# Optimization experiments

Hardware: AMD Instinct MI355X
Metric: run time of the kernel (lower is better)

Reference implementation:

```python
import jax, jax.numpy as jnp
import numpy as np

E = 19   # electrodes
H = 32   # lstm hidden dim per direction


def setup_inputs() -> dict:
    key = jax.random.key(0)
    ks = jax.random.split(key, 8)
    B, T = 64, 2048
    s = 1.0 / np.sqrt(H)  # PyTorch LSTM/Linear init scale
    u = lambda k, shp: jax.random.uniform(k, shp, jnp.float32, -s, s)
    return {
        "x": jax.random.normal(ks[0], (B, T, E), jnp.float32),
        # per-electrode, per-direction LSTM params (input_dim=1 so w_ih is a vector per gate block)
        "w_ih": u(ks[1], (E, 2, 4 * H)),          # [E, dir, 4H]
        "w_hh": u(ks[2], (E, 2, 4 * H, H)),       # [E, dir, 4H, H]
        "b_ih": u(ks[3], (E, 2, 4 * H)),
        "b_hh": u(ks[4], (E, 2, 4 * H)),
        "ln_gamma": jnp.ones((E, 2 * H), jnp.float32),
        "ln_beta": jnp.zeros((E, 2 * H), jnp.float32),
        "fc_w": u(ks[5], (1, 2 * H)),
        "fc_b": u(ks[6], (1,)),
    }


def reference(x, w_ih, w_hh, b_ih, b_hh, ln_gamma, ln_beta, fc_w, fc_b):
    B, T, E_ = x.shape
    # dir 0 = forward time, dir 1 = reversed time (bidirectional)
    xs = jnp.stack([x, x[:, ::-1, :]], axis=-1)      # [B, T, E, 2]
    xs = jnp.moveaxis(xs, 1, 0)                      # [T, B, E, 2]
    b = b_ih + b_hh                                  # [E, 2, 4H]

    h0 = jnp.zeros((B, E_, 2, H), x.dtype)
    c0 = jnp.zeros_like(h0)

    def step(carry, xt):
        h, c = carry
        # xt: [B, E, 2] scalar input per electrode/direction (input_dim == 1)
        gates = xt[..., None] * w_ih + jnp.einsum('bedh,edgh->bedg', h, w_hh) + b
        i, f, g, o = jnp.split(gates, 4, axis=-1)    # PyTorch gate order i,f,g,o
        c = jax.nn.sigmoid(f) * c + jax.nn.sigmoid(i) * jnp.tanh(g)
        h = jax.nn.sigmoid(o) * jnp.tanh(c)
        return (h, c), None

    (hT, _), _ = jax.lax.scan(step, (h0, c0), xs)
    # final hidden: dir0 = fwd at t=T-1 (hn[-2]), dir1 = bwd at t=0 (hn[-1]); concat features
    out = hT.reshape(B, E_, 2 * H)                   # [B, E, 64]

    # per-electrode LayerNorm over the 64-dim feature
    mu = out.mean(-1, keepdims=True)
    var = out.var(-1, keepdims=True)
    out = (out - mu) / jnp.sqrt(var + 1e-5) * ln_gamma + ln_beta

    pooled = out.mean(axis=1)                        # mean over electrodes -> [B, 64]
    logits = pooled @ fc_w.T + fc_b                  # [B, 1]
    return logits[:, 0]
```

## Files before the change

### kernel.cpp

```cpp
#include <hip/hip_runtime.h>
#include <math.h>
#include <stdint.h>

#define E_N 19
#define H_N 32
#define T_N 2048
#define B_N 64
#define G_N 128
#define XCHUNK 64
#define LOG2E 1.4426950408889634f

typedef _Float16 half2_t __attribute__((ext_vector_type(2)));

__device__ __forceinline__ float sigm_rcp(float e) {
    return __builtin_amdgcn_rcpf(1.0f + e);
}

__global__ __launch_bounds__(64)
__attribute__((amdgpu_waves_per_eu(3, 3)))
void lstm_chain_kernel(
    const float* __restrict__ x,
    const float* __restrict__ w_ih,
    const float* __restrict__ w_hh,
    const float* __restrict__ b_ih,
    const float* __restrict__ b_hh,
    float* __restrict__ hT)
{
    const int lane  = threadIdx.x;
    const int chain = blockIdx.x;
    const int b  = chain / (E_N * 2);
    const int ed = chain - b * (E_N * 2);
    const int e  = ed >> 1;
    const int d  = ed & 1;
    const int j    = lane & 31;
    const int half = lane >> 5;

    const int r1 = j + 32 * half;
    const int r2 = j + 64 + 32 * half;

    const float* wr1 = w_hh + ((size_t)ed * G_N + r1) * H_N;
    const float* wr2 = w_hh + ((size_t)ed * G_N + r2) * H_N;
    uint32_t w1p[16], w2p[16];
    #pragma unroll
    for (int m = 0; m < 16; ++m) {
        float2 v1 = ((const float2*)wr1)[m];
        float2 v2 = ((const float2*)wr2)[m];
        half2_t p1 = { (_Float16)v1.x, (_Float16)v1.y };
        half2_t p2 = { (_Float16)v2.x, (_Float16)v2.y };
        w1p[m] = __builtin_bit_cast(uint32_t, p1);
        w2p[m] = __builtin_bit_cast(uint32_t, p2);
    }

    const float wih1  = w_ih[(size_t)ed * G_N + r1];
    const float wih2  = w_ih[(size_t)ed * G_N + r2];
    const float bias1 = b_ih[(size_t)ed * G_N + r1] + b_hh[(size_t)ed * G_N + r1];
    const float bias2 = b_ih[(size_t)ed * G_N + r2] + b_hh[(size_t)ed * G_N + r2];

    const float K2 = half ? (-LOG2E) : (-2.0f * LOG2E);
    const float A2 = half ?  1.0f :  2.0f;
    const float B2 = half ?  0.0f : -1.0f;

    __shared__ __align__(16) uint16_t hbuf[64];
    __shared__ float xbuf[XCHUNK];

    if (lane < 32) hbuf[lane] = 0;
    float c = 0.0f;
    float h = 0.0f;

    const float* xbase = x + (size_t)b * T_N * E_N + e;
    const int hwr = j + 32 * (1 - half);

    for (int t0 = 0; t0 < T_N; t0 += XCHUNK) {
        #pragma unroll
        for (int m = 0; m < 16; ++m) {
            asm volatile("" : "+v"(w1p[m]), "+v"(w2p[m]));
        }

        const int tt    = t0 + lane;
        const int tphys = d ? (T_N - 1 - tt) : tt;
        xbuf[lane] = xbase[(size_t)tphys * E_N];

        #pragma unroll 1
        for (int tl = 0; tl < XCHUNK; ++tl) {
            const uint4 q0 = ((const uint4*)hbuf)[0];
            const uint4 q1 = ((const uint4*)hbuf)[1];
            const uint4 q2 = ((const uint4*)hbuf)[2];
            const uint4 q3 = ((const uint4*)hbuf)[3];
            const float sx = xbuf[tl];

            uint32_t hp[16];
            hp[0]=q0.x; hp[1]=q0.y; hp[2]=q0.z; hp[3]=q0.w;
            hp[4]=q1.x; hp[5]=q1.y; hp[6]=q1.z; hp[7]=q1.w;
            hp[8]=q2.x; hp[9]=q2.y; hp[10]=q2.z; hp[11]=q2.w;
            hp[12]=q3.x; hp[13]=q3.y; hp[14]=q3.z; hp[15]=q3.w;

            float a1 = fmaf(sx, wih1, bias1), a1b = 0.0f;
            float a2 = fmaf(sx, wih2, bias2), a2b = 0.0f;
            #pragma unroll
            for (int m = 0; m < 8; ++m) {
                a1  = __builtin_amdgcn_fdot2(__builtin_bit_cast(half2_t, hp[m]),
                                             __builtin_bit_cast(half2_t, w1p[m]),   a1,  false);
                a1b = __builtin_amdgcn_fdot2(__builtin_bit_cast(half2_t, hp[m+8]),
                                             __builtin_bit_cast(half2_t, w1p[m+8]), a1b, false);
                a2  = __builtin_amdgcn_fdot2(__builtin_bit_cast(half2_t, hp[m]),
                                             __builtin_bit_cast(half2_t, w2p[m]),   a2,  false);
                a2b = __builtin_amdgcn_fdot2(__builtin_bit_cast(half2_t, hp[m+8]),
                                             __builtin_bit_cast(half2_t, w2p[m+8]), a2b, false);
            }
            const float g1 = a1 + a1b;
            const float g2 = a2 + a2b;

            const float act1 = sigm_rcp(__builtin_amdgcn_exp2f(g1 * (-LOG2E)));
            const float act2 = fmaf(A2, sigm_rcp(__builtin_amdgcn_exp2f(g2 * K2)), B2);

            const float ig  = act1 * act2;
            const float igx = __shfl_xor(ig, 32);

            c = fmaf(act1, c, igx);
            const float tc = fmaf(2.0f, sigm_rcp(
                __builtin_amdgcn_exp2f(c * (-2.0f * LOG2E))), -1.0f);
            h = act2 * tc;

            hbuf[hwr] = __builtin_bit_cast(uint16_t, (_Float16)h);
        }
    }

    if (half) {
        hT[((size_t)(b * E_N + e) * 2 + d) * H_N + j] = h;
    }
}

__global__ __launch_bounds__(64) void head_kernel(
    const float* __restrict__ hT,
    const float* __restrict__ ln_gamma,
    const float* __restrict__ ln_beta,
    const float* __restrict__ fc_w,
    const float* __restrict__ fc_b,
    float* __restrict__ out)
{
    const int b = blockIdx.x;
    const int f = threadIdx.x;

    float acc = 0.0f;
    for (int e = 0; e < E_N; ++e) {
        const float v = hT[(size_t)(b * E_N + e) * 64 + f];
        float s = v, s2 = v * v;
        #pragma unroll
        for (int off = 32; off > 0; off >>= 1) {
            s  += __shfl_xor(s,  off);
            s2 += __shfl_xor(s2, off);
        }
        const float mean = s * (1.0f / 64.0f);
        const float var  = s2 * (1.0f / 64.0f) - mean * mean;
        const float inv  = rsqrtf(var + 1e-5f);
        acc += (v - mean) * inv * ln_gamma[e * 64 + f] + ln_beta[e * 64 + f];
    }
    float contrib = (acc * (1.0f / (float)E_N)) * fc_w[f];
    #pragma unroll
    for (int off = 32; off > 0; off >>= 1) contrib += __shfl_xor(contrib, off);
    if (f == 0) out[b] = contrib + fc_b[0];
}

extern "C" void kernel_launch(void* const* d_in, const int* in_sizes, int n_in,
                              void* d_out, int out_size, void* d_ws, size_t ws_size,
                              hipStream_t stream) {
    const float* x        = (const float*)d_in[0];
    const float* w_ih     = (const float*)d_in[1];
    const float* w_hh     = (const float*)d_in[2];
    const float* b_ih     = (const float*)d_in[3];
    const float* b_hh     = (const float*)d_in[4];
    const float* ln_gamma = (const float*)d_in[5];
    const float* ln_beta  = (const float*)d_in[6];
    const float* fc_w     = (const float*)d_in[7];
    const float* fc_b     = (const float*)d_in[8];
    float* out = (float*)d_out;
    float* hT  = (float*)d_ws;

    lstm_chain_kernel<<<B_N * E_N * 2, 64, 0, stream>>>(x, w_ih, w_hh, b_ih, b_hh, hT);
    head_kernel<<<B_N, 64, 0, stream>>>(hT, ln_gamma, ln_beta, fc_w, fc_b, out);
}
```

Before: 894.9 us.

## Pack both LSTM directions into one wave, each lane computing all four gates

Each 64-lane block now handles one (batch, electrode) pair, with lanes 0-31 running the forward direction and lanes 32-63 the backward direction, instead of one block per direction that split the gate rows across two half-waves. Each lane now holds all four gate rows (64 packed fp16 weight registers) and computes i, f, g, o itself. This removes the cross-half shuffle from every timestep and halves the block count. In exchange each lane does twice the dot-product work per step, register pressure rises, and the waves_per_eu hint is dropped. The x chunk is also halved and the next chunk is prefetched into a register.

```diff
diff --git a/kernel.cpp b/kernel.cpp
--- a/kernel.cpp
+++ b/kernel.cpp
@@ -7,7 +7,7 @@
 #define T_N 2048
 #define B_N 64
 #define G_N 128
-#define XCHUNK 64
+#define XCHUNK 32
 #define LOG2E 1.4426950408889634f
 
 typedef _Float16 half2_t __attribute__((ext_vector_type(2)));
@@ -17,7 +17,6 @@
 }
 
 __global__ __launch_bounds__(64)
-__attribute__((amdgpu_waves_per_eu(3, 3)))
 void lstm_chain_kernel(
     const float* __restrict__ x,
     const float* __restrict__ w_ih,
@@ -26,67 +25,69 @@
     const float* __restrict__ b_hh,
     float* __restrict__ hT)
 {
-    const int lane  = threadIdx.x;
-    const int chain = blockIdx.x;
-    const int b  = chain / (E_N * 2);
-    const int ed = chain - b * (E_N * 2);
-    const int e  = ed >> 1;
-    const int d  = ed & 1;
+    const int lane = threadIdx.x;
+    const int be   = blockIdx.x;
+    const int b    = be / E_N;
+    const int e    = be - b * E_N;
     const int j    = lane & 31;
     const int half = lane >> 5;
+    const int ed   = e * 2 + half;
 
-    const int r1 = j + 32 * half;
-    const int r2 = j + 64 + 32 * half;
-
-    const float* wr1 = w_hh + ((size_t)ed * G_N + r1) * H_N;
-    const float* wr2 = w_hh + ((size_t)ed * G_N + r2) * H_N;
-    uint32_t w1p[16], w2p[16];
+    const float* wbase = w_hh + (size_t)ed * G_N * H_N;
+    uint32_t wp[4][16];
     #pragma unroll
-    for (int m = 0; m < 16; ++m) {
-        float2 v1 = ((const float2*)wr1)[m];
-        float2 v2 = ((const float2*)wr2)[m];
-        half2_t p1 = { (_Float16)v1.x, (_Float16)v1.y };
-        half2_t p2 = { (_Float16)v2.x, (_Float16)v2.y };
-        w1p[m] = __builtin_bit_cast(uint32_t, p1);
-        w2p[m] = __builtin_bit_cast(uint32_t, p2);
+    for (int r = 0; r < 4; ++r) {
+        const float* wr = wbase + (size_t)(j + 32 * r) * H_N;
+        #pragma unroll
+        for (int m = 0; m < 16; ++m) {
+            float2 v = ((const float2*)wr)[m];
+            half2_t p = { (_Float16)v.x, (_Float16)v.y };
+            wp[r][m] = __builtin_bit_cast(uint32_t, p);
+        }
+    }
+    float wih[4], bias[4];
+    #pragma unroll
+    for (int r = 0; r < 4; ++r) {
+        const int row = j + 32 * r;
+        wih[r]  = w_ih[(size_t)ed * G_N + row];
+        bias[r] = b_ih[(size_t)ed * G_N + row] + b_hh[(size_t)ed * G_N + row];
     }
 
-    const float wih1  = w_ih[(size_t)ed * G_N + r1];
-    const float wih2  = w_ih[(size_t)ed * G_N + r2];
-    const float bias1 = b_ih[(size_t)ed * G_N + r1] + b_hh[(size_t)ed * G_N + r1];
-    const float bias2 = b_ih[(size_t)ed * G_N + r2] + b_hh[(size_t)ed * G_N + r2];
+    __shared__ __align__(16) uint16_t hbuf[64];
+    __shared__ float xbuf[64];
 
-    const float K2 = half ? (-LOG2E) : (-2.0f * LOG2E);
-    const float A2 = half ?  1.0f :  2.0f;
-    const float B2 = half ?  0.0f : -1.0f;
-
-    __shared__ __align__(16) uint16_t hbuf[64];
-    __shared__ float xbuf[XCHUNK];
-
-    if (lane < 32) hbuf[lane] = 0;
-    float c = 0.0f;
-    float h = 0.0f;
+    hbuf[lane] = 0;
+    float c = 0.0f, h = 0.0f;
 
     const float* xbase = x + (size_t)b * T_N * E_N + e;
-    const int hwr = j + 32 * (1 - half);
+
+    float xreg;
+    {
+        const int tphys = half ? (T_N - 1 - j) : j;
+        xreg = xbase[(size_t)tphys * E_N];
+    }
 
     for (int t0 = 0; t0 < T_N; t0 += XCHUNK) {
         #pragma unroll
-        for (int m = 0; m < 16; ++m) {
-            asm volatile("" : "+v"(w1p[m]), "+v"(w2p[m]));
+        for (int r = 0; r < 4; ++r)
+            #pragma unroll
+            for (int m = 0; m < 16; ++m)
+                asm volatile("" : "+v"(wp[r][m]));
+
+        xbuf[lane] = xreg;
+        if (t0 + XCHUNK < T_N) {
+            const int tn    = t0 + XCHUNK + j;
+            const int tphys = half ? (T_N - 1 - tn) : tn;
+            xreg = xbase[(size_t)tphys * E_N];
         }
-
-        const int tt    = t0 + lane;
-        const int tphys = d ? (T_N - 1 - tt) : tt;
-        xbuf[lane] = xbase[(size_t)tphys * E_N];
 
         #pragma unroll 1
         for (int tl = 0; tl < XCHUNK; ++tl) {
-            const uint4 q0 = ((const uint4*)hbuf)[0];
-            const uint4 q1 = ((const uint4*)hbuf)[1];
-            const uint4 q2 = ((const uint4*)hbuf)[2];
-            const uint4 q3 = ((const uint4*)hbuf)[3];
-            const float sx = xbuf[tl];
+            const uint4 q0 = ((const uint4*)hbuf)[half * 4 + 0];
+            const uint4 q1 = ((const uint4*)hbuf)[half * 4 + 1];
+            const uint4 q2 = ((const uint4*)hbuf)[half * 4 + 2];
+            const uint4 q3 = ((const uint4*)hbuf)[half * 4 + 3];
+            const float sx = xbuf[(half << 5) + tl];
 
             uint32_t hp[16];
             hp[0]=q0.x; hp[1]=q0.y; hp[2]=q0.z; hp[3]=q0.w;
@@ -94,40 +95,45 @@
             hp[8]=q2.x; hp[9]=q2.y; hp[10]=q2.z; hp[11]=q2.w;
             hp[12]=q3.x; hp[13]=q3.y; hp[14]=q3.z; hp[15]=q3.w;
 
-            float a1 = fmaf(sx, wih1, bias1), a1b = 0.0f;
-            float a2 = fmaf(sx, wih2, bias2), a2b = 0.0f;
+            float acc[4], accb[4];
+            #pragma unroll
+            for (int r = 0; r < 4; ++r) {
+                acc[r]  = fmaf(sx, wih[r], bias[r]);
+                accb[r] = 0.0f;
+            }
             #pragma unroll
             for (int m = 0; m < 8; ++m) {
-                a1  = __builtin_amdgcn_fdot2(__builtin_bit_cast(half2_t, hp[m]),
-                                             __builtin_bit_cast(half2_t, w1p[m]),   a1,  false);
-                a1b = __builtin_amdgcn_fdot2(__builtin_bit_cast(half2_t, hp[m+8]),
-                                             __builtin_bit_cast(half2_t, w1p[m+8]), a1b, false);
-                a2  = __builtin_amdgcn_fdot2(__builtin_bit_cast(half2_t, hp[m]),
-                                             __builtin_bit_cast(half2_t, w2p[m]),   a2,  false);
-                a2b = __builtin_amdgcn_fdot2(__builtin_bit_cast(half2_t, hp[m+8]),
-                                             __builtin_bit_cast(half2_t, w2p[m+8]), a2b, false);
+                #pragma unroll
+                for (int r = 0; r < 4; ++r) {
+                    acc[r]  = __builtin_amdgcn_fdot2(
+                        __builtin_bit_cast(half2_t, hp[m]),
+                        __builtin_bit_cast(half2_t, wp[r][m]),   acc[r],  false);
+                    accb[r] = __builtin_amdgcn_fdot2(
+                        __builtin_bit_cast(half2_t, hp[m + 8]),
+                        __builtin_bit_cast(half2_t, wp[r][m + 8]), accb[r], false);
+                }
             }
-            const float g1 = a1 + a1b;
-            const float g2 = a2 + a2b;
+            const float gi = acc[0] + accb[0];
+            const float gf = acc[1] + accb[1];
+            const float gg = acc[2] + accb[2];
+            const float go = acc[3] + accb[3];
 
-            const float act1 = sigm_rcp(__builtin_amdgcn_exp2f(g1 * (-LOG2E)));
-            const float act2 = fmaf(A2, sigm_rcp(__builtin_amdgcn_exp2f(g2 * K2)), B2);
+            const float si = sigm_rcp(__builtin_amdgcn_exp2f(gi * (-LOG2E)));
+            const float sf = sigm_rcp(__builtin_amdgcn_exp2f(gf * (-LOG2E)));
+            const float tg = fmaf(2.0f, sigm_rcp(
+                __builtin_amdgcn_exp2f(gg * (-2.0f * LOG2E))), -1.0f);
+            const float so = sigm_rcp(__builtin_amdgcn_exp2f(go * (-LOG2E)));
 
-            const float ig  = act1 * act2;
-            const float igx = __shfl_xor(ig, 32);
-
-            c = fmaf(act1, c, igx);
+            c = fmaf(sf, c, si * tg);
             const float tc = fmaf(2.0f, sigm_rcp(
                 __builtin_amdgcn_exp2f(c * (-2.0f * LOG2E))), -1.0f);
-            h = act2 * tc;
+            h = so * tc;
 
-            hbuf[hwr] = __builtin_bit_cast(uint16_t, (_Float16)h);
+            hbuf[lane] = __builtin_bit_cast(uint16_t, (_Float16)h);
         }
     }
 
-    if (half) {
-        hT[((size_t)(b * E_N + e) * 2 + d) * H_N + j] = h;
-    }
+    hT[((size_t)(b * E_N + e) * 2 + half) * H_N + j] = h;
 }
 
 __global__ __launch_bounds__(64) void head_kernel(
@@ -176,6 +182,6 @@
     float* out = (float*)d_out;
     float* hT  = (float*)d_ws;
 
-    lstm_chain_kernel<<<B_N * E_N * 2, 64, 0, stream>>>(x, w_ih, w_hh, b_ih, b_hh, hT);
+    lstm_chain_kernel<<<B_N * E_N, 64, 0, stream>>>(x, w_ih, w_hh, b_ih, b_hh, hT);
     head_kernel<<<B_N, 64, 0, stream>>>(hT, ln_gamma, ln_beta, fc_w, fc_b, out);
 }
```

Measured after the change: 973.4 us. 1.09x slower.

## Replace LDS hidden-state exchange with DPP/permlane register broadcasts

Applied to the files above, without the earlier changes.

Removes the shared-memory round trip for the hidden state each timestep. Each lane now assembles the other lanes' fp16 h values through a tree of DPP moves plus a shuffle, with the recurrent weights pre-permuted to match that order. The cross-half gate exchange uses permlane32_swap instead of a shuffle, and the x inputs are held in a register and read per step with readlane, with the next chunk prefetched. This adds about 16 DPP ops per step to the dependent chain, in exchange for dropping the LDS write, the wait and the four 16-byte reads.

```diff
diff --git a/kernel.cpp b/kernel.cpp
--- a/kernel.cpp
+++ b/kernel.cpp
@@ -11,10 +11,17 @@
 #define LOG2E 1.4426950408889634f
 
 typedef _Float16 half2_t __attribute__((ext_vector_type(2)));
+typedef int v2i_t __attribute__((ext_vector_type(2)));
 
 __device__ __forceinline__ float sigm_rcp(float e) {
     return __builtin_amdgcn_rcpf(1.0f + e);
 }
+
+#define DPP_XOR1  0xB1
+#define DPP_XOR2  0x4E
+#define DPP_HMIRR 0x141
+#define DPP_MIRR  0x140
+#define MOVDPP(x, ctrl) ((uint32_t)__builtin_amdgcn_mov_dpp((int)(x), (ctrl), 0xF, 0xF, false))
 
 __global__ __launch_bounds__(64)
 __attribute__((amdgpu_waves_per_eu(3, 3)))
@@ -32,21 +39,23 @@
     const int ed = chain - b * (E_N * 2);
     const int e  = ed >> 1;
     const int d  = ed & 1;
-    const int j    = lane & 31;
+    const int a    = lane & 31;
     const int half = lane >> 5;
 
-    const int r1 = j + 32 * half;
-    const int r2 = j + 64 + 32 * half;
+    const int r1 = a + 32 * half;
+    const int r2 = a + 64 + 32 * half;
+
+    const int XT0[16] = {0,1,2,3, 7,6,5,4, 15,14,13,12, 8,9,10,11};
 
     const float* wr1 = w_hh + ((size_t)ed * G_N + r1) * H_N;
     const float* wr2 = w_hh + ((size_t)ed * G_N + r2) * H_N;
     uint32_t w1p[16], w2p[16];
     #pragma unroll
     for (int m = 0; m < 16; ++m) {
-        float2 v1 = ((const float2*)wr1)[m];
-        float2 v2 = ((const float2*)wr2)[m];
-        half2_t p1 = { (_Float16)v1.x, (_Float16)v1.y };
-        half2_t p2 = { (_Float16)v2.x, (_Float16)v2.y };
+        const int k0 = a ^ XT0[m];
+        const int k1 = k0 ^ 16;
+        half2_t p1 = { (_Float16)wr1[k0], (_Float16)wr1[k1] };
+        half2_t p2 = { (_Float16)wr2[k0], (_Float16)wr2[k1] };
         w1p[m] = __builtin_bit_cast(uint32_t, p1);
         w2p[m] = __builtin_bit_cast(uint32_t, p2);
     }
@@ -60,73 +69,93 @@
     const float A2 = half ?  1.0f :  2.0f;
     const float B2 = half ?  0.0f : -1.0f;
 
-    __shared__ __align__(16) uint16_t hbuf[64];
-    __shared__ float xbuf[XCHUNK];
-
-    if (lane < 32) hbuf[lane] = 0;
     float c = 0.0f;
     float h = 0.0f;
+    float h_all = 0.0f;
 
     const float* xbase = x + (size_t)b * T_N * E_N + e;
-    const int hwr = j + 32 * (1 - half);
+    float xcur, xnext = 0.0f;
+    {
+        const int tp = d ? (T_N - 1 - lane) : lane;
+        xcur = xbase[(size_t)tp * E_N];
+    }
 
     for (int t0 = 0; t0 < T_N; t0 += XCHUNK) {
         #pragma unroll
         for (int m = 0; m < 16; ++m) {
             asm volatile("" : "+v"(w1p[m]), "+v"(w2p[m]));
         }
-
-        const int tt    = t0 + lane;
-        const int tphys = d ? (T_N - 1 - tt) : tt;
-        xbuf[lane] = xbase[(size_t)tphys * E_N];
+        if (t0 + XCHUNK < T_N) {
+            const int tn = t0 + XCHUNK + lane;
+            const int tp = d ? (T_N - 1 - tn) : tn;
+            xnext = xbase[(size_t)tp * E_N];
+        }
 
         #pragma unroll 1
         for (int tl = 0; tl < XCHUNK; ++tl) {
-            const uint4 q0 = ((const uint4*)hbuf)[0];
-            const uint4 q1 = ((const uint4*)hbuf)[1];
-            const uint4 q2 = ((const uint4*)hbuf)[2];
-            const uint4 q3 = ((const uint4*)hbuf)[3];
-            const float sx = xbuf[tl];
-
-            uint32_t hp[16];
-            hp[0]=q0.x; hp[1]=q0.y; hp[2]=q0.z; hp[3]=q0.w;
-            hp[4]=q1.x; hp[5]=q1.y; hp[6]=q1.z; hp[7]=q1.w;
-            hp[8]=q2.x; hp[9]=q2.y; hp[10]=q2.z; hp[11]=q2.w;
-            hp[12]=q3.x; hp[13]=q3.y; hp[14]=q3.z; hp[15]=q3.w;
-
-            float a1 = fmaf(sx, wih1, bias1), a1b = 0.0f;
-            float a2 = fmaf(sx, wih2, bias2), a2b = 0.0f;
-            #pragma unroll
-            for (int m = 0; m < 8; ++m) {
-                a1  = __builtin_amdgcn_fdot2(__builtin_bit_cast(half2_t, hp[m]),
-                                             __builtin_bit_cast(half2_t, w1p[m]),   a1,  false);
-                a1b = __builtin_amdgcn_fdot2(__builtin_bit_cast(half2_t, hp[m+8]),
-                                             __builtin_bit_cast(half2_t, w1p[m+8]), a1b, false);
-                a2  = __builtin_amdgcn_fdot2(__builtin_bit_cast(half2_t, hp[m]),
-                                             __builtin_bit_cast(half2_t, w2p[m]),   a2,  false);
-                a2b = __builtin_amdgcn_fdot2(__builtin_bit_cast(half2_t, hp[m+8]),
-                                             __builtin_bit_cast(half2_t, w2p[m+8]), a2b, false);
-            }
-            const float g1 = a1 + a1b;
-            const float g2 = a2 + a2b;
+            const float sx = __builtin_bit_cast(float,
+                __builtin_amdgcn_readlane(__builtin_bit_cast(int, xcur), tl));
+
+            const float hx16 = __shfl_xor(h_all, 16);
+            const uint32_t hb0 = (uint32_t)__builtin_bit_cast(uint16_t, (_Float16)h_all);
+            const uint32_t hb1 = (uint32_t)__builtin_bit_cast(uint16_t, (_Float16)hx16);
+            const uint32_t R0  = (hb1 << 16) | hb0;
+            const uint32_t R1  = MOVDPP(R0, DPP_XOR1);
+            const uint32_t R2  = MOVDPP(R0, DPP_XOR2);
+            const uint32_t R3  = MOVDPP(R1, DPP_XOR2);
+            const uint32_t R4  = MOVDPP(R0, DPP_HMIRR);
+            const uint32_t R5  = MOVDPP(R1, DPP_HMIRR);
+            const uint32_t R6  = MOVDPP(R2, DPP_HMIRR);
+            const uint32_t R7  = MOVDPP(R3, DPP_HMIRR);
+            const uint32_t R8  = MOVDPP(R0, DPP_MIRR);
+            const uint32_t R9  = MOVDPP(R1, DPP_MIRR);
+            const uint32_t R10 = MOVDPP(R2, DPP_MIRR);
+            const uint32_t R11 = MOVDPP(R3, DPP_MIRR);
+            const uint32_t R12 = MOVDPP(R4, DPP_MIRR);
+            const uint32_t R13 = MOVDPP(R5, DPP_MIRR);
+            const uint32_t R14 = MOVDPP(R6, DPP_MIRR);
+            const uint32_t R15 = MOVDPP(R7, DPP_MIRR);
+
+            #define FD(Rr, wv, acc) \
+                acc = __builtin_amdgcn_fdot2(__builtin_bit_cast(half2_t, Rr), \
+                                             __builtin_bit_cast(half2_t, wv), acc, false)
+            float s10 = fmaf(sx, wih1, bias1), s11 = 0.0f, s12 = 0.0f, s13 = 0.0f;
+            float s20 = fmaf(sx, wih2, bias2), s21 = 0.0f, s22 = 0.0f, s23 = 0.0f;
+            FD(R0,  w1p[0],  s10); FD(R4,  w1p[4],  s11); FD(R8,  w1p[8],  s12); FD(R12, w1p[12], s13);
+            FD(R1,  w1p[1],  s10); FD(R5,  w1p[5],  s11); FD(R9,  w1p[9],  s12); FD(R13, w1p[13], s13);
+            FD(R2,  w1p[2],  s10); FD(R6,  w1p[6],  s11); FD(R10, w1p[10], s12); FD(R14, w1p[14], s13);
+            FD(R3,  w1p[3],  s10); FD(R7,  w1p[7],  s11); FD(R11, w1p[11], s12); FD(R15, w1p[15], s13);
+            FD(R0,  w2p[0],  s20); FD(R4,  w2p[4],  s21); FD(R8,  w2p[8],  s22); FD(R12, w2p[12], s23);
+            FD(R1,  w2p[1],  s20); FD(R5,  w2p[5],  s21); FD(R9,  w2p[9],  s22); FD(R13, w2p[13], s23);
+            FD(R2,  w2p[2],  s20); FD(R6,  w2p[6],  s21); FD(R10, w2p[10], s22); FD(R14, w2p[14], s23);
+            FD(R3,  w2p[3],  s20); FD(R7,  w2p[7],  s21); FD(R11, w2p[11], s22); FD(R15, w2p[15], s23);
+            #undef FD
+            const float g1 = (s10 + s11) + (s12 + s13);
+            const float g2 = (s20 + s21) + (s22 + s23);
 
             const float act1 = sigm_rcp(__builtin_amdgcn_exp2f(g1 * (-LOG2E)));
             const float act2 = fmaf(A2, sigm_rcp(__builtin_amdgcn_exp2f(g2 * K2)), B2);
 
             const float ig  = act1 * act2;
-            const float igx = __shfl_xor(ig, 32);
+            const int igb   = __builtin_bit_cast(int, ig);
+            const v2i_t pr  = __builtin_amdgcn_permlane32_swap(igb, igb, false, false);
+            const float igx = __builtin_bit_cast(float, pr.x ^ pr.y ^ igb);
 
             c = fmaf(act1, c, igx);
             const float tc = fmaf(2.0f, sigm_rcp(
                 __builtin_amdgcn_exp2f(c * (-2.0f * LOG2E))), -1.0f);
             h = act2 * tc;
 
-            hbuf[hwr] = __builtin_bit_cast(uint16_t, (_Float16)h);
-        }
+            const int hb      = __builtin_bit_cast(int, h);
+            const v2i_t ph    = __builtin_amdgcn_permlane32_swap(hb, hb, false, false);
+            const float hpart = __builtin_bit_cast(float, ph.x ^ ph.y ^ hb);
+            h_all = half ? h : hpart;
+        }
+        xcur = xnext;
     }
 
     if (half) {
-        hT[((size_t)(b * E_N + e) * 2 + d) * H_N + j] = h;
+        hT[((size_t)(b * E_N + e) * 2 + d) * H_N + a] = h;
     }
 }
 
```

Result: slower. 1.189 ms (+32.9%).
